# Optimization experiments

Measured on AMD Instinct MI355X. Metric: run time of the kernel, lower is better.

## Reference

```python
import jax, jax.numpy as jnp
import numpy as np
from jax import lax

B = 8          # batch
IMG = 224      # image size
PATCH = 16     # patch size / stride
D = 384        # embed_dim = d_model = d_inner (expand=1)
DEPTH = 24     # number of blocks
N = 16         # d_state
K = 4          # d_conv
R = 24         # dt_rank = ceil(D/16)
H = D * 4 * 2 // 3   # SwiGLU hidden = 1024
L = (IMG // PATCH) ** 2  # 196 tokens


def setup_inputs() -> dict:
    ks = iter(jax.random.split(jax.random.key(0), 40))
    def rn(shape, s=0.02):
        return jax.random.normal(next(ks), shape, jnp.float32) * s
    inp = {}
    inp["x"] = jax.random.normal(next(ks), (B, 3, IMG, IMG), jnp.float32)
    inp["patch_w"] = rn((D, 3, PATCH, PATCH))
    inp["patch_b"] = jnp.zeros((D,), jnp.float32)
    inp["norm1_w"] = jnp.ones((DEPTH, D), jnp.float32)
    inp["norm1_b"] = jnp.zeros((DEPTH, D), jnp.float32)
    inp["in_proj_w"] = rn((DEPTH, 2 * D, D))
    inp["conv_w"] = rn((DEPTH, D, K), 0.1)
    inp["conv_b"] = jnp.zeros((DEPTH, D), jnp.float32)
    inp["x_proj_w"] = rn((DEPTH, R + 2 * N, D))
    inp["dt_proj_w"] = rn((DEPTH, D, R), 0.1)
    inp["dt_proj_b"] = rn((DEPTH, D), 0.1)
    # S4D-real init: A = -exp(A_log), A_log = log(1..N)
    inp["A_log"] = jnp.tile(jnp.log(jnp.arange(1, N + 1, dtype=jnp.float32))[None, None, :], (DEPTH, D, 1))
    inp["D_skip"] = jnp.ones((DEPTH, D), jnp.float32)
    inp["out_proj_w"] = rn((DEPTH, D, D))
    inp["norm2_w"] = jnp.ones((DEPTH, D), jnp.float32)
    inp["norm2_b"] = jnp.zeros((DEPTH, D), jnp.float32)
    inp["w1_w"] = rn((DEPTH, H, D)); inp["w1_b"] = jnp.zeros((DEPTH, H), jnp.float32)
    inp["w2_w"] = rn((DEPTH, H, D)); inp["w2_b"] = jnp.zeros((DEPTH, H), jnp.float32)
    inp["w3_w"] = rn((DEPTH, D, H)); inp["w3_b"] = jnp.zeros((DEPTH, D), jnp.float32)
    inp["normf_w"] = jnp.ones((D,), jnp.float32)
    inp["normf_b"] = jnp.zeros((D,), jnp.float32)
    return inp


def _ln(x, w, b, eps=1e-5):
    m = x.mean(-1, keepdims=True)
    v = jnp.mean((x - m) ** 2, axis=-1, keepdims=True)
    return (x - m) / jnp.sqrt(v + eps) * w + b


def _mamba(x, in_w, cw, cb, xp_w, dtw, dtb, a_log, d_skip, ow):
    # x: [B, L, D]; Mamba with expand=1, bimamba 'none'
    bsz, seq, _ = x.shape
    xz = jnp.einsum('bld,ed->ble', x, in_w)        # [B, L, 2D]
    xc, z = jnp.split(xz, 2, axis=-1)
    # causal depthwise conv1d, kernel K, padding K-1, truncated to L
    xpd = jnp.pad(xc, ((0, 0), (K - 1, 0), (0, 0)))
    xconv = sum(xpd[:, k:k + seq, :] * cw[:, k] for k in range(K)) + cb
    xa = jax.nn.silu(xconv)
    dbc = jnp.einsum('bld,ed->ble', xa, xp_w)      # [B, L, R+2N]
    dt = jax.nn.softplus(jnp.einsum('blr,dr->bld', dbc[..., :R], dtw) + dtb)  # [B, L, D]
    Bm = dbc[..., R:R + N]                         # [B, L, N]
    Cm = dbc[..., R + N:]                          # [B, L, N]
    A = -jnp.exp(a_log)                            # [D, N]

    def step(h, t):
        dt_t, B_t, C_t, x_t = t                    # [B,D],[B,N],[B,N],[B,D]
        h = h * jnp.exp(dt_t[..., None] * A) + (dt_t * x_t)[..., None] * B_t[:, None, :]
        return h, jnp.einsum('bdn,bn->bd', h, C_t)

    h0 = jnp.zeros((bsz, D, N), x.dtype)
    _, ys = lax.scan(step, h0, (dt.transpose(1, 0, 2), Bm.transpose(1, 0, 2),
                                Cm.transpose(1, 0, 2), xa.transpose(1, 0, 2)))
    y = ys.transpose(1, 0, 2) + d_skip * xa
    y = y * jax.nn.silu(z)
    return jnp.einsum('bld,ed->ble', y, ow)


def _forward(x, patch_w, patch_b, norm1_w, norm1_b, in_proj_w, conv_w, conv_b,
             x_proj_w, dt_proj_w, dt_proj_b, A_log, D_skip, out_proj_w,
             norm2_w, norm2_b, w1_w, w1_b, w2_w, w2_b, w3_w, w3_b, normf_w, normf_b):
    p = lax.conv_general_dilated(x, patch_w, (PATCH, PATCH), 'VALID',
                                 dimension_numbers=('NCHW', 'OIHW', 'NCHW'))
    p = p + patch_b[None, :, None, None]
    h = p.reshape(p.shape[0], D, -1).transpose(0, 2, 1)   # [B, L, D]
    for i in range(DEPTH):
        h = h + _mamba(_ln(h, norm1_w[i], norm1_b[i]), in_proj_w[i], conv_w[i], conv_b[i],
                       x_proj_w[i], dt_proj_w[i], dt_proj_b[i], A_log[i], D_skip[i], out_proj_w[i])
        hn = _ln(h, norm2_w[i], norm2_b[i])
        hid = jax.nn.silu(hn @ w1_w[i].T + w1_b[i]) * (hn @ w2_w[i].T + w2_b[i])
        h = h + hid @ w3_w[i].T + w3_b[i]
    return _ln(h, normf_w, normf_b)


def reference(x, patch_w, patch_b, norm1_w, norm1_b, in_proj_w, conv_w, conv_b,
              x_proj_w, dt_proj_w, dt_proj_b, A_log, D_skip, out_proj_w,
              norm2_w, norm2_b, w1_w, w1_b, w2_w, w2_b, w3_w, w3_b, normf_w, normf_b):
    return _forward(x, patch_w, patch_b, norm1_w, norm1_b, in_proj_w, conv_w, conv_b,
                    x_proj_w, dt_proj_w, dt_proj_b, A_log, D_skip, out_proj_w,
                    norm2_w, norm2_b, w1_w, w1_b, w2_w, w2_b, w3_w, w3_b, normf_w, normf_b)
```

## Files before the change

kernel.cpp:

```cpp
#include <hip/hip_runtime.h>
#include <math.h>

#define BB 8
#define LL 196
#define DD 384
#define NDEPTH 24
#define NST 16
#define RRANK 24
#define HHID 1024
#define MROWS (BB*LL)
#define NCH 28
#define CHL 7

typedef float f32x4 __attribute__((ext_vector_type(4)));
typedef short s16x8 __attribute__((ext_vector_type(8)));
typedef short s16x4 __attribute__((ext_vector_type(4)));
typedef __bf16 b16x8 __attribute__((ext_vector_type(8)));
typedef unsigned short u16;
typedef unsigned int u32;

#if defined(__has_builtin)
#  if __has_builtin(__builtin_amdgcn_global_load_lds)
#    define HAS_GLL 1
#  endif
#endif
#ifndef HAS_GLL
#  define HAS_GLL 0
#endif

__device__ __forceinline__ float sigmoidf_(float x){ return 1.f/(1.f+__expf(-x)); }

__device__ __forceinline__ u16 f2bf(float f){
    u32 u = __builtin_bit_cast(u32, f);
    u32 r = (u + 0x7fffu + ((u >> 16) & 1u)) >> 16;
    return (u16)r;
}
__device__ __forceinline__ float bf2f(u16 v){
    u32 u = ((u32)v) << 16;
    return __builtin_bit_cast(float, u);
}

__device__ __forceinline__ void gll16(const u16* g, void* lds){
#if HAS_GLL
    __builtin_amdgcn_global_load_lds(
        (const __attribute__((address_space(1))) unsigned int*)g,
        (__attribute__((address_space(3))) unsigned int*)lds, 16, 0, 0);
#endif
}

template<int N> __device__ __forceinline__ void waitbar(){
    if constexpr (N==0) asm volatile("s_waitcnt vmcnt(0) lgkmcnt(0)\ns_barrier" ::: "memory");
    else if constexpr (N==4) asm volatile("s_waitcnt vmcnt(4) lgkmcnt(0)\ns_barrier" ::: "memory");
    else if constexpr (N==8) asm volatile("s_waitcnt vmcnt(8) lgkmcnt(0)\ns_barrier" ::: "memory");
    else asm volatile("s_waitcnt vmcnt(0) lgkmcnt(0)\ns_barrier" ::: "memory");
    __builtin_amdgcn_sched_barrier(0);
}
__device__ __forceinline__ void bar_release(){
    asm volatile("s_waitcnt lgkmcnt(0)\ns_barrier" ::: "memory");
    __builtin_amdgcn_sched_barrier(0);
}

template<typename V>
__device__ __forceinline__ auto mfma_try(V a, V b, f32x4 c, int)
    -> decltype(__builtin_amdgcn_mfma_f32_16x16x32_bf16(a, b, c, 0, 0, 0))
{ return __builtin_amdgcn_mfma_f32_16x16x32_bf16(a, b, c, 0, 0, 0); }

template<typename V>
__device__ __forceinline__ f32x4 mfma_try(V a, V b, f32x4 c, long)
{
    return __builtin_amdgcn_mfma_f32_16x16x32_bf16(
        __builtin_bit_cast(b16x8, a), __builtin_bit_cast(b16x8, b), c, 0, 0, 0);
}
__device__ __forceinline__ f32x4 mfma_bf16(s16x8 a, s16x8 b, f32x4 c){ return mfma_try(a, b, c, 0); }

__global__ __launch_bounds__(64) void ln_k(const float* __restrict__ X,
    const float* __restrict__ w, const float* __restrict__ b, float* __restrict__ Y)
{
    int row = blockIdx.x;
    int lane = threadIdx.x;
    const float* x = X + (size_t)row*DD;
    float v[6]; float s=0.f, s2=0.f;
    #pragma unroll
    for (int j=0;j<6;j++){ float t = x[lane + j*64]; v[j]=t; s+=t; s2+=t*t; }
    #pragma unroll
    for (int o=32;o>=1;o>>=1){ s += __shfl_xor(s,o); s2 += __shfl_xor(s2,o); }
    float m = s*(1.f/DD);
    float var = s2*(1.f/DD) - m*m;
    float rstd = rsqrtf(var + 1e-5f);
    #pragma unroll
    for (int j=0;j<6;j++){
        int c = lane + j*64;
        Y[(size_t)row*DD + c] = (v[j]-m)*rstd*w[c] + b[c];
    }
}

__global__ void gather_k(const float* __restrict__ x, u16* __restrict__ P)
{
    int idx = blockIdx.x*blockDim.x + threadIdx.x;
    if (idx >= MROWS*768) return;
    int k = idx % 768;
    int bl = idx / 768;
    int l = bl % LL;
    int b = bl / LL;
    int c = k >> 8;
    int rem = k & 255;
    int dy = rem >> 4, dx = rem & 15;
    int py = l / 14, px = l % 14;
    P[idx] = f2bf(x[(((size_t)b*3 + c)*224 + (py*16+dy))*224 + (px*16+dx)]);
}

__device__ __forceinline__ int swz(int row, int chunk){
    return (row << 7) + ((chunk ^ (row & 7)) << 4);
}

template<int EPI, bool WB, int CFG, int PRO, int K>
__global__ __launch_bounds__(256) void mgemm_k(
    const u16* __restrict__ A, const float* __restrict__ Af,
    const float* __restrict__ lnw, const float* __restrict__ lnb,
    const void* __restrict__ W1v, const void* __restrict__ W2v,
    const float* __restrict__ bias1, const float* __restrict__ bias2,
    float* __restrict__ Cf, u16* __restrict__ Cb,
    int M, int N)
{
    constexpr int  BM   = (CFG==1)?32:16;
    constexpr int  FM   = (CFG==2)?1:2;
    constexpr int  FN   = 2;
    constexpr int  NAR  = (BM+31)/32;
    constexpr bool DUAL = (EPI==4);
    constexpr bool RES  = (EPI==2 || EPI==3);
    constexpr int  ABY  = BM*128;
    constexpr int  BBY  = 128*128;
    constexpr bool ASY  = WB && (HAS_GLL==1);
    constexpr int  NKT  = K >> 6;
    constexpr int  NLW  = DUAL ? 8 : 4;
    __shared__ __attribute__((aligned(16))) char sm[2*ABY + 2*BBY + (DUAL ? 2*BBY : 0)];
    char* A0 = sm;          char* A1 = sm + ABY;
    char* B0 = sm + 2*ABY;  char* B1 = B0 + BBY;
    char* C0 = B1 + BBY;    char* C1 = C0 + BBY;

    const int tid = threadIdx.x;
    const int row0 = blockIdx.y * BM;
    const int col0 = blockIdx.x << 7;
    const int w = tid >> 6, lane = tid & 63;
    const int wn  = w;
    const int lr = lane & 15, lk = lane >> 4;
    const int ar0 = tid >> 3, ac8 = tid & 7;
    const bool apart = (CFG != 2) || (tid < 128);

    const u16*   W1b = (const u16*)W1v;
    const u16*   W2b = (const u16*)W2v;
    const float* W1f = (const float*)W1v;
    const float* W2f = (const float*)W2v;

    f32x4 acc [FM][FN] = {};
    f32x4 acc2[FM][FN] = {};

    float cres[FM][FN][4];
    if (RES){
        #pragma unroll
        for (int n=0;n<FN;n++){
            int gc = col0 + wn*32 + n*16 + lr;
            #pragma unroll
            for (int m=0;m<FM;m++){
                #pragma unroll
                for (int r=0;r<4;r++){
                    int gr = row0 + m*16 + lk*4 + r;
                    cres[m][n][r] = (gc < N && gr < M) ? Cf[(size_t)gr*N + gc] : 0.f;
                }
            }
        }
    }

    s16x8 aval[NAR];
    s16x8 bval[4], b2val[4];
    float4 bvf[8], b2vf[8];
    s16x8 lnr[(PRO==1)?NKT:1];

    if (PRO == 1 && apart){
        const float* xrow = Af + (size_t)(row0 + ar0)*DD;
        float4 va[6], vb[6];
        float s = 0.f, s2 = 0.f;
        #pragma unroll
        for (int j=0;j<6;j++){
            va[j] = *(const float4*)(xrow + j*64 + ac8*8);
            vb[j] = *(const float4*)(xrow + j*64 + ac8*8 + 4);
            s  += va[j].x+va[j].y+va[j].z+va[j].w + vb[j].x+vb[j].y+vb[j].z+vb[j].w;
            s2 += va[j].x*va[j].x+va[j].y*va[j].y+va[j].z*va[j].z+va[j].w*va[j].w
                + vb[j].x*vb[j].x+vb[j].y*vb[j].y+vb[j].z*vb[j].z+vb[j].w*vb[j].w;
        }
        #pragma unroll
        for (int o=1;o<8;o<<=1){ s += __shfl_xor(s,o); s2 += __shfl_xor(s2,o); }
        float m = s*(1.f/DD);
        float rstd = rsqrtf(s2*(1.f/DD) - m*m + 1e-5f);
        #pragma unroll
        for (int j=0;j<6;j++){
            int c0 = j*64 + ac8*8;
            float4 w0 = *(const float4*)(lnw + c0);
            float4 w1 = *(const float4*)(lnw + c0 + 4);
            float4 b0 = *(const float4*)(lnb + c0);
            float4 b1 = *(const float4*)(lnb + c0 + 4);
            s16x8 ov;
            ov[0]=(short)f2bf((va[j].x-m)*rstd*w0.x+b0.x);
            ov[1]=(short)f2bf((va[j].y-m)*rstd*w0.y+b0.y);
            ov[2]=(short)f2bf((va[j].z-m)*rstd*w0.z+b0.z);
            ov[3]=(short)f2bf((va[j].w-m)*rstd*w0.w+b0.w);
            ov[4]=(short)f2bf((vb[j].x-m)*rstd*w1.x+b1.x);
            ov[5]=(short)f2bf((vb[j].y-m)*rstd*w1.y+b1.y);
            ov[6]=(short)f2bf((vb[j].z-m)*rstd*w1.z+b1.z);
            ov[7]=(short)f2bf((vb[j].w-m)*rstd*w1.w+b1.w);
            if (j < NKT) lnr[j] = ov;
        }
    }

    auto stageAsync = [&](int kt, char* bA, char* bB, char* bC){
        const int lhi = lane >> 3, llo = lane & 7;
        const int colel = (kt << 6) + ((llo ^ lhi) << 3);
        if (PRO == 0){
            constexpr int ACH = BM/8;
            #pragma unroll
            for (int ci = w; ci < ACH; ci += 4){
                int gr = row0 + ci*8 + lhi;
                gll16(A + (size_t)gr*K + colel, bA + ci*1024);
            }
        }
        #pragma unroll
        for (int i=0;i<4;i++){
            int ci = w*4 + i;
            int gb = col0 + ci*8 + lhi;
            gll16(W1b + (size_t)gb*K + colel, bB + ci*1024);
        }
        if (DUAL){
            #pragma unroll
            for (int i=0;i<4;i++){
                int ci = w*4 + i;
                int gb = col0 + ci*8 + lhi;
                gll16(W2b + (size_t)gb*K + colel, bC + ci*1024);
            }
        }
    };

    auto loadT = [&](int kt){
        const int kb = kt << 6;
        if (PRO == 0 && apart){
            #pragma unroll
            for (int i=0;i<NAR;i++){
                int gr = row0 + i*32 + ar0;
                if (gr < M) aval[i] = *(const s16x8*)(A + (size_t)gr*K + kb + ac8*8);
                else        aval[i] = s16x8{0,0,0,0,0,0,0,0};
            }
        }
        if (WB){
            #pragma unroll
            for (int i=0;i<4;i++){
                int gb = col0 + i*32 + ar0;
                if (gb < N) bval[i] = *(const s16x8*)(W1b + (size_t)gb*K + kb + ac8*8);
                else        bval[i] = s16x8{0,0,0,0,0,0,0,0};
            }
            if (DUAL){
                #pragma unroll
                for (int i=0;i<4;i++){
                    int gb = col0 + i*32 + ar0;
                    if (gb < N) b2val[i] = *(const s16x8*)(W2b + (size_t)gb*K + kb + ac8*8);
                    else        b2val[i] = s16x8{0,0,0,0,0,0,0,0};
                }
            }
        } else {
            #pragma unroll
            for (int i=0;i<8;i++){
                int ss = i*256 + tid;
                int r = ss >> 4, q = ss & 15;
                int gb = col0 + r;
                if (gb < N) bvf[i] = *(const float4*)(W1f + (size_t)gb*K + kb + q*4);
                else        bvf[i] = float4{0,0,0,0};
            }
            if (DUAL){
                #pragma unroll
                for (int i=0;i<8;i++){
                    int ss = i*256 + tid;
                    int r = ss >> 4, q = ss & 15;
                    int gb = col0 + r;
                    if (gb < N) b2vf[i] = *(const float4*)(W2f + (size_t)gb*K + kb + q*4);
                    else        b2vf[i] = float4{0,0,0,0};
                }
            }
        }
    };
    auto writeT = [&](char* bA, char* bB, char* bC){
        if (PRO == 0 && apart){
            #pragma unroll
            for (int i=0;i<NAR;i++)
                *(s16x8*)(bA + swz(i*32 + ar0, ac8)) = aval[i];
        }
        if (WB){
            #pragma unroll
            for (int i=0;i<4;i++)
                *(s16x8*)(bB + swz(i*32 + ar0, ac8)) = bval[i];
            if (DUAL){
                #pragma unroll
                for (int i=0;i<4;i++)
                    *(s16x8*)(bC + swz(i*32 + ar0, ac8)) = b2val[i];
            }
        } else {
            #pragma unroll
            for (int i=0;i<8;i++){
                int ss = i*256 + tid;
                int r = ss >> 4, q = ss & 15;
                float4 v = bvf[i];
                s16x4 cv = { (short)f2bf(v.x), (short)f2bf(v.y), (short)f2bf(v.z), (short)f2bf(v.w) };
                int off = (r << 7) + (((q >> 1) ^ (r & 7)) << 4) + ((q & 1) << 3);
                *(s16x4*)(bB + off) = cv;
            }
            if (DUAL){
                #pragma unroll
                for (int i=0;i<8;i++){
                    int ss = i*256 + tid;
                    int r = ss >> 4, q = ss & 15;
                    float4 v = b2vf[i];
                    s16x4 cv = { (short)f2bf(v.x), (short)f2bf(v.y), (short)f2bf(v.z), (short)f2bf(v.w) };
                    int off = (r << 7) + (((q >> 1) ^ (r & 7)) << 4) + ((q & 1) << 3);
                    *(s16x4*)(bC + off) = cv;
                }
            }
        }
    };

    auto compute = [&](char* cA, char* cB, char* cC){
        #pragma unroll
        for (int ks=0; ks<2; ks++){
            s16x8 af[FM], bfr[FN];
            #pragma unroll
            for (int m=0;m<FM;m++)
                af[m] = *(const s16x8*)(cA + swz(m*16 + lr, ks*4 + lk));
            #pragma unroll
            for (int n=0;n<FN;n++)
                bfr[n] = *(const s16x8*)(cB + swz(wn*32 + n*16 + lr, ks*4 + lk));
            #pragma unroll
            for (int m=0;m<FM;m++)
                #pragma unroll
                for (int n=0;n<FN;n++)
                    acc[m][n] = mfma_bf16(af[m], bfr[n], acc[m][n]);
            if (DUAL){
                s16x8 b2r[FN];
                #pragma unroll
                for (int n=0;n<FN;n++)
                    b2r[n] = *(const s16x8*)(cC + swz(wn*32 + n*16 + lr, ks*4 + lk));
                #pragma unroll
                for (int m=0;m<FM;m++)
                    #pragma unroll
                    for (int n=0;n<FN;n++)
                        acc2[m][n] = mfma_bf16(af[m], b2r[n], acc2[m][n]);
            }
        }
    };

    if (ASY){
        stageAsync(0, A0, B0, C0);
        if (NKT > 1) stageAsync(1, A1, B1, C1);
        if (PRO == 1 && apart){
            *(s16x8*)(A0 + swz(ar0, ac8)) = lnr[0];
            if (NKT > 1) *(s16x8*)(A1 + swz(ar0, ac8)) = lnr[(1 < NKT) ? 1 : 0];
        }
        if (NKT > 1) waitbar<NLW>(); else waitbar<0>();
        #pragma unroll
        for (int kt=0; kt<NKT; kt++){
            if (kt & 1) compute(A1, B1, C1);
            else        compute(A0, B0, C0);
            if (kt+1 < NKT){
                bar_release();
                if (kt+2 < NKT){
                    char* rA = (kt&1)?A1:A0; char* rB = (kt&1)?B1:B0; char* rC = (kt&1)?C1:C0;
                    stageAsync(kt+2, rA, rB, rC);
                    if (PRO == 1 && apart)
                        *(s16x8*)(rA + swz(ar0, ac8)) = lnr[(kt+2 < NKT) ? (kt+2) : 0];
                    waitbar<NLW>();
                } else {
                    waitbar<0>();
                }
            }
        }
    } else {
        loadT(0); writeT(A0, B0, C0);
        if (PRO == 1 && apart) *(s16x8*)(A0 + swz(ar0, ac8)) = lnr[0];
        __syncthreads();
        #pragma unroll
        for (int kt=0; kt<NKT; kt++){
            const bool more = (kt+1 < NKT);
            char* nA = (kt&1)?A0:A1; char* nB = (kt&1)?B0:B1; char* nC = (kt&1)?C0:C1;
            if (more){
                loadT(kt+1);
                if (PRO == 1 && apart) *(s16x8*)(nA + swz(ar0, ac8)) = lnr[(kt+1 < NKT) ? (kt+1) : 0];
            }
            if (kt & 1) compute(A1, B1, C1);
            else        compute(A0, B0, C0);
            if (more) writeT(nA, nB, nC);
            __syncthreads();
        }
    }

    #pragma unroll
    for (int n=0;n<FN;n++){
        int gc = col0 + wn*32 + n*16 + lr;
        if (gc >= N) continue;
        float b1 = 0.f, b2 = 0.f;
        if (EPI==1||EPI==3||EPI==4) b1 = bias1[gc];
        if (EPI==4) b2 = bias2[gc];
        #pragma unroll
        for (int m=0;m<FM;m++){
            #pragma unroll
            for (int r=0;r<4;r++){
                int gr = row0 + m*16 + lk*4 + r;
                if (gr >= M) continue;
                float v = acc[m][n][r];
                if (EPI==1||EPI==3) v += b1;
                if (RES) v += cres[m][n][r];
                if (EPI==4){
                    float v1 = v + b1;
                    float v2 = acc2[m][n][r] + b2;
                    Cb[(size_t)gr*N + gc] = f2bf(v1 * sigmoidf_(v1) * v2);
                } else if (EPI==6){
                    Cb[(size_t)gr*N + gc] = f2bf(v);
                } else {
                    Cf[(size_t)gr*N + gc] = v;
                }
            }
        }
    }
}

__global__ void cvtw_k(const float* __restrict__ s, u16* __restrict__ d, int n)
{
    int i = blockIdx.x*blockDim.x + threadIdx.x;
    int idx = i*4;
    if (idx + 4 <= n){
        float4 v = *(const float4*)(s + idx);
        s16x4 cv = { (short)f2bf(v.x), (short)f2bf(v.y), (short)f2bf(v.z), (short)f2bf(v.w) };
        *(s16x4*)(d + idx) = cv;
    } else {
        for (int j=idx;j<n;j++) d[j] = f2bf(s[j]);
    }
}

__global__ __launch_bounds__(384) void scanA_k(
    const float* __restrict__ Wx, const u16* __restrict__ xzb,
    const float* __restrict__ cw, const float* __restrict__ cb,
    const float* __restrict__ dtw, const float* __restrict__ dtb,
    const float* __restrict__ a_log,
    float* __restrict__ Pout, float* __restrict__ Sout,
    float2* __restrict__ dtxv, float* __restrict__ dbc)
{
    __shared__ float xaS[CHL][DD+4];
    __shared__ float Ds[CHL][56];
    int b = blockIdx.x / NCH;
    int c = blockIdx.x % NCH;
    int d = threadIdx.x;

    float cwr[4];
    #pragma unroll
    for (int k=0;k<4;k++) cwr[k] = cw[d*4+k];
    float cbv = cb[d];
    int l0 = c*CHL;
    float p3=0.f, p2=0.f, p1=0.f;
    if (l0 >= 3) p3 = bf2f(xzb[(size_t)(b*LL+l0-3)*768 + d]);
    if (l0 >= 2) p2 = bf2f(xzb[(size_t)(b*LL+l0-2)*768 + d]);
    if (l0 >= 1) p1 = bf2f(xzb[(size_t)(b*LL+l0-1)*768 + d]);
    float xv[CHL];
    #pragma unroll
    for (int j=0;j<CHL;j++){
        int row = b*LL + l0 + j;
        float cur = bf2f(xzb[(size_t)row*768 + d]);
        float a = cbv;
        a = fmaf(p3, cwr[0], a); a = fmaf(p2, cwr[1], a);
        a = fmaf(p1, cwr[2], a); a = fmaf(cur, cwr[3], a);
        p3 = p2; p2 = p1; p1 = cur;
        xv[j] = a * sigmoidf_(a);
        xaS[j][d] = xv[j];
    }
    __syncthreads();

    for (int t = d; t < CHL*56; t += 384){
        int q = t / CHL, j = t - q*CHL;
        const float* Wr = Wx + (size_t)q*DD;
        float accd = 0.f;
        #pragma unroll 8
        for (int dd=0; dd<DD; dd+=4){
            float4 wv = *(const float4*)(Wr + dd);
            accd = fmaf(xaS[j][dd],   wv.x, accd);
            accd = fmaf(xaS[j][dd+1], wv.y, accd);
            accd = fmaf(xaS[j][dd+2], wv.z, accd);
            accd = fmaf(xaS[j][dd+3], wv.w, accd);
        }
        Ds[j][q] = accd;
        dbc[(size_t)(b*LL + l0 + j)*56 + q] = accd;
    }
    __syncthreads();

    float dtwr[RRANK];
    #pragma unroll
    for (int r=0;r<RRANK;r++) dtwr[r] = dtw[d*RRANK + r];
    float dtbv = dtb[d];
    float Aa[NST];
    #pragma unroll
    for (int n=0;n<NST;n++) Aa[n] = -__expf(a_log[d*NST+n]);
    float hst[NST], P[NST];
    #pragma unroll
    for (int n=0;n<NST;n++){ hst[n]=0.f; P[n]=1.f; }
    #pragma unroll
    for (int j=0;j<CHL;j++){
        int row = b*LL + l0 + j;
        float t = dtbv;
        #pragma unroll
        for (int r=0;r<RRANK;r++) t = fmaf(dtwr[r], Ds[j][r], t);
        float dtv = (t > 20.f) ? t : log1pf(__expf(t));
        dtxv[(size_t)row*DD + d] = float2{dtv, xv[j]};
        float du = dtv*xv[j];
        #pragma unroll
        for (int n=0;n<NST;n++){
            float e = __expf(dtv*Aa[n]);
            hst[n] = fmaf(hst[n], e, du*Ds[j][24+n]);
            P[n] *= e;
        }
    }
    size_t base = ((size_t)(b*NCH + c)*DD + d)*NST;
    #pragma unroll
    for (int n=0;n<NST;n++){ Pout[base+n]=P[n]; Sout[base+n]=hst[n]; }
}

__global__ __launch_bounds__(256) void scanB_k(
    const float* __restrict__ P, const float* __restrict__ S,
    float* __restrict__ Hin)
{
    int t = blockIdx.x*blockDim.x + threadIdx.x;
    if (t >= BB*DD*NST) return;
    int n = t % NST;
    int d = (t / NST) % DD;
    int b = t / (NST*DD);
    float h = 0.f;
    for (int c=0; c<NCH; c++){
        size_t idx = ((size_t)(b*NCH + c)*DD + d)*NST + n;
        Hin[idx] = h;
        h = fmaf(P[idx], h, S[idx]);
    }
}

__global__ __launch_bounds__(384) void scanC_k(
    const float* __restrict__ dbc, const float2* __restrict__ dtxv,
    const u16* __restrict__ xzb, const float* __restrict__ a_log,
    const float* __restrict__ Hin,
    const float* __restrict__ dskip,
    u16* __restrict__ yg)
{
    int b = blockIdx.x / NCH;
    int c = blockIdx.x % NCH;
    int d = threadIdx.x;
    __shared__ float Ds[CHL][56];
    for (int t = threadIdx.x; t < CHL*56; t += 384){
        int j = t/56, q = t%56;
        Ds[j][q] = dbc[(size_t)(b*LL + c*CHL + j)*56 + q];
    }
    __syncthreads();
    float hst[NST];
    size_t hb = ((size_t)(b*NCH + c)*DD + d)*NST;
    #pragma unroll
    for (int n=0;n<NST;n++) hst[n] = Hin[hb+n];
    float Aa[NST];
    #pragma unroll
    for (int n=0;n<NST;n++) Aa[n] = -__expf(a_log[d*NST+n]);
    float dsk = dskip[d];
    int l0 = c*CHL;
    #pragma unroll
    for (int j=0;j<CHL;j++){
        int row = b*LL + l0 + j;
        float2 dx = dtxv[(size_t)row*DD + d];
        float dtv = dx.x, xv = dx.y;
        float du = dtv*xv;
        float y = 0.f;
        #pragma unroll
        for (int n=0;n<NST;n++){
            float e = __expf(dtv*Aa[n]);
            hst[n] = fmaf(hst[n], e, du*Ds[j][24+n]);
            y = fmaf(hst[n], Ds[j][40+n], y);
        }
        float zv = bf2f(xzb[(size_t)row*768 + 384 + d]);
        float g = zv * sigmoidf_(zv);
        yg[(size_t)row*DD + d] = f2bf((y + dsk*xv)*g);
    }
}

template<int EPI, int CFG, int PRO, int K>
static void mg(bool wb, dim3 g, hipStream_t s,
               const void* A, const float* Af, const float* lnw, const float* lnb,
               const void* Wb, const void* Wf, const void* W2b, const void* W2f,
               const float* b1, const float* b2, float* Cf, u16* Cb,
               int M, int N)
{
    if (wb) mgemm_k<EPI,true ,CFG,PRO,K><<<g,256,0,s>>>((const u16*)A, Af, lnw, lnb, Wb, W2b, b1, b2, Cf, Cb, M, N);
    else    mgemm_k<EPI,false,CFG,PRO,K><<<g,256,0,s>>>((const u16*)A, Af, lnw, lnb, Wf, W2f, b1, b2, Cf, Cb, M, N);
}

extern "C" void kernel_launch(void* const* d_in, const int* in_sizes, int n_in,
                              void* d_out, int out_size, void* d_ws, size_t ws_size,
                              hipStream_t stream)
{
    const float* x         = (const float*)d_in[0];
    const float* patch_w   = (const float*)d_in[1];
    const float* patch_b   = (const float*)d_in[2];
    const float* norm1_w   = (const float*)d_in[3];
    const float* norm1_b   = (const float*)d_in[4];
    const float* in_proj_w = (const float*)d_in[5];
    const float* conv_w    = (const float*)d_in[6];
    const float* conv_b    = (const float*)d_in[7];
    const float* x_proj_w  = (const float*)d_in[8];
    const float* dt_w      = (const float*)d_in[9];
    const float* dt_b      = (const float*)d_in[10];
    const float* A_log     = (const float*)d_in[11];
    const float* D_skip    = (const float*)d_in[12];
    const float* out_w     = (const float*)d_in[13];
    const float* norm2_w   = (const float*)d_in[14];
    const float* norm2_b   = (const float*)d_in[15];
    const float* w1_w      = (const float*)d_in[16];
    const float* w1_b      = (const float*)d_in[17];
    const float* w2_w      = (const float*)d_in[18];
    const float* w2_b      = (const float*)d_in[19];
    const float* w3_w      = (const float*)d_in[20];
    const float* w3_b      = (const float*)d_in[21];
    const float* normf_w   = (const float*)d_in[22];
    const float* normf_b   = (const float*)d_in[23];

    char* wsb = (char*)d_ws;
    size_t o = 0;
    auto take = [&](size_t bytes) -> char* {
        char* p = wsb + o;
        o += (bytes + 255) & ~(size_t)255;
        return p;
    };

    float* h    = (float*)take((size_t)602112*4);
    float* dbc  = (float*)take((size_t)87808*4);
    float* Pb   = (float*)take((size_t)BB*NCH*DD*NST*4);
    float* Sb   = (float*)take((size_t)BB*NCH*DD*NST*4);
    float* Hi   = (float*)take((size_t)BB*NCH*DD*NST*4);
    float2* dtxv= (float2*)take((size_t)MROWS*DD*8);
    u16*  xzb   = (u16*)take((size_t)1204224*2);
    u16*  yg    = (u16*)take((size_t)602112*2);
    u16*  hid   = (u16*)take((size_t)1605632*2);
    u16*  patches = hid;

    const size_t NPW = 294912, NIN = 7077888, NOUT = 3538944,
                 NW1 = 9437184, NW2 = 9437184, NW3 = 9437184;
    u16* wcP = (u16*)take(NPW*2);
    u16* wcI = (u16*)take(NIN*2);
    u16* wcO = (u16*)take(NOUT*2);
    u16* wc1 = (u16*)take(NW1*2);
    u16* wc2 = (u16*)take(NW2*2);
    u16* wc3 = (u16*)take(NW3*2);
    bool wb = (ws_size >= o);

    if (wb){
        cvtw_k<<<(int)((NPW/4+255)/256), 256, 0, stream>>>(patch_w, wcP, (int)NPW);
        cvtw_k<<<(int)((NIN/4+255)/256), 256, 0, stream>>>(in_proj_w, wcI, (int)NIN);
        cvtw_k<<<(int)((NOUT/4+255)/256),256, 0, stream>>>(out_w, wcO, (int)NOUT);
        cvtw_k<<<(int)((NW1/4+255)/256), 256, 0, stream>>>(w1_w, wc1, (int)NW1);
        cvtw_k<<<(int)((NW2/4+255)/256), 256, 0, stream>>>(w2_w, wc2, (int)NW2);
        cvtw_k<<<(int)((NW3/4+255)/256), 256, 0, stream>>>(w3_w, wc3, (int)NW3);
    }

    const int GY32 = MROWS/32;
    const int GY16 = MROWS/16;

    gather_k<<<(MROWS*768+255)/256, 256, 0, stream>>>(x, patches);
    mg<1,2,0,768>(wb, dim3(3,GY16), stream, patches, nullptr, nullptr, nullptr,
              wcP, patch_w, nullptr, nullptr, patch_b, nullptr, h, nullptr, MROWS, DD);

    for (int i=0;i<NDEPTH;i++){
        mg<6,1,1,384>(wb, dim3(6,GY32), stream, nullptr, h, norm1_w + i*DD, norm1_b + i*DD,
                  wcI + (size_t)i*768*DD, in_proj_w + (size_t)i*768*DD, nullptr, nullptr,
                  nullptr, nullptr, nullptr, xzb, MROWS, 768);
        scanA_k<<<BB*NCH, 384, 0, stream>>>(x_proj_w + (size_t)i*56*DD, xzb,
                                            conv_w + i*DD*4, conv_b + i*DD,
                                            dt_w + (size_t)i*DD*RRANK, dt_b + i*DD,
                                            A_log + (size_t)i*DD*NST, Pb, Sb, dtxv, dbc);
        scanB_k<<<(BB*DD*NST+255)/256, 256, 0, stream>>>(Pb, Sb, Hi);
        scanC_k<<<BB*NCH, 384, 0, stream>>>(dbc, dtxv, xzb, A_log + (size_t)i*DD*NST,
                                            Hi, D_skip + i*DD, yg);
        mg<2,2,0,384>(wb, dim3(3,GY16), stream, yg, nullptr, nullptr, nullptr,
                  wcO + (size_t)i*DD*DD, out_w + (size_t)i*DD*DD, nullptr, nullptr,
                  nullptr, nullptr, h, nullptr, MROWS, DD);
        mg<4,1,1,384>(wb, dim3(8,GY32), stream, nullptr, h, norm2_w + i*DD, norm2_b + i*DD,
                  wc1 + (size_t)i*HHID*DD, w1_w + (size_t)i*HHID*DD,
                  wc2 + (size_t)i*HHID*DD, w2_w + (size_t)i*HHID*DD,
                  w1_b + i*HHID, w2_b + i*HHID, nullptr, hid, MROWS, HHID);
        mg<3,2,0,1024>(wb, dim3(3,GY16), stream, hid, nullptr, nullptr, nullptr,
                  wc3 + (size_t)i*DD*HHID, w3_w + (size_t)i*DD*HHID, nullptr, nullptr,
                  w3_b + i*DD, nullptr, h, nullptr, MROWS, DD);
    }

    ln_k<<<MROWS, 64, 0, stream>>>(h, normf_w, normf_b, (float*)d_out);
}
```

Baseline: 1.963 ms.

## Fuse out_proj GEMM into scan output kernel with fp32 FMA

Removes the separate out_proj MFMA GEMM launch by having each scanC block keep its 7-row y*gate tile in shared memory and compute the 384x384 projection with scalar fp32 FMAs, adding the result straight into the residual h. Out_proj weights are pre-transposed into an interleaved fp32 layout so each thread reads float4 weights coalesced. This saves a launch and the bf16 yg round trip through global memory. In exchange, every block re-reads the full fp32 weight matrix, and the projection runs on vector ALUs instead of matrix cores.

```diff
diff --git a/kernel.cpp b/kernel.cpp
--- a/kernel.cpp
+++ b/kernel.cpp
@@ -440,6 +440,17 @@
     }
 }
 
+__global__ void cvtP_k(const float* __restrict__ s, float* __restrict__ d)
+{
+    int idx = blockIdx.x*blockDim.x + threadIdx.x;
+    if (idx >= NDEPTH*DD*DD) return;
+    int q   = idx & 3;
+    int e   = (idx >> 2) % DD;
+    int dd4 = ((idx >> 2) / DD) % (DD/4);
+    int L   = idx / (DD*DD);
+    d[idx] = s[(size_t)L*DD*DD + (size_t)e*DD + dd4*4 + q];
+}
+
 __global__ __launch_bounds__(384) void scanA_k(
     const float* __restrict__ Wx, const u16* __restrict__ xzb,
     const float* __restrict__ cw, const float* __restrict__ cb,
@@ -542,17 +553,19 @@
     }
 }
 
+template<int FUSE>
 __global__ __launch_bounds__(384) void scanC_k(
     const float* __restrict__ dbc, const float2* __restrict__ dtxv,
     const u16* __restrict__ xzb, const float* __restrict__ a_log,
     const float* __restrict__ Hin,
-    const float* __restrict__ dskip,
-    u16* __restrict__ yg)
-{
+    const float* __restrict__ dskip, const float* __restrict__ Wp,
+    float* __restrict__ h, u16* __restrict__ yg)
+{
+    __shared__ float ygS[CHL][DD+4];
+    __shared__ float Ds[CHL][56];
     int b = blockIdx.x / NCH;
     int c = blockIdx.x % NCH;
     int d = threadIdx.x;
-    __shared__ float Ds[CHL][56];
     for (int t = threadIdx.x; t < CHL*56; t += 384){
         int j = t/56, q = t%56;
         Ds[j][q] = dbc[(size_t)(b*LL + c*CHL + j)*56 + q];
@@ -582,7 +595,32 @@
         }
         float zv = bf2f(xzb[(size_t)row*768 + 384 + d]);
         float g = zv * sigmoidf_(zv);
-        yg[(size_t)row*DD + d] = f2bf((y + dsk*xv)*g);
+        float yv = (y + dsk*xv)*g;
+        if (FUSE) ygS[j][d] = yv;
+        else      yg[(size_t)row*DD + d] = f2bf(yv);
+    }
+    if (FUSE){
+        __syncthreads();
+        float o[CHL];
+        #pragma unroll
+        for (int j=0;j<CHL;j++) o[j] = 0.f;
+        #pragma unroll 4
+        for (int dd4=0; dd4<DD/4; dd4++){
+            float4 wv = *(const float4*)(Wp + ((size_t)dd4*DD + d)*4);
+            int dd = dd4*4;
+            #pragma unroll
+            for (int j=0;j<CHL;j++){
+                o[j] = fmaf(ygS[j][dd],   wv.x, o[j]);
+                o[j] = fmaf(ygS[j][dd+1], wv.y, o[j]);
+                o[j] = fmaf(ygS[j][dd+2], wv.z, o[j]);
+                o[j] = fmaf(ygS[j][dd+3], wv.w, o[j]);
+            }
+        }
+        #pragma unroll
+        for (int j=0;j<CHL;j++){
+            size_t idx = (size_t)(b*LL + l0 + j)*DD + d;
+            h[idx] += o[j];
+        }
     }
 }
 
@@ -647,21 +685,21 @@
 
     const size_t NPW = 294912, NIN = 7077888, NOUT = 3538944,
                  NW1 = 9437184, NW2 = 9437184, NW3 = 9437184;
-    u16* wcP = (u16*)take(NPW*2);
-    u16* wcI = (u16*)take(NIN*2);
-    u16* wcO = (u16*)take(NOUT*2);
-    u16* wc1 = (u16*)take(NW1*2);
-    u16* wc2 = (u16*)take(NW2*2);
-    u16* wc3 = (u16*)take(NW3*2);
+    u16*   wcP = (u16*)take(NPW*2);
+    u16*   wcI = (u16*)take(NIN*2);
+    u16*   wc1 = (u16*)take(NW1*2);
+    u16*   wc2 = (u16*)take(NW2*2);
+    u16*   wc3 = (u16*)take(NW3*2);
+    float* wpO = (float*)take(NOUT*4);
     bool wb = (ws_size >= o);
 
     if (wb){
         cvtw_k<<<(int)((NPW/4+255)/256), 256, 0, stream>>>(patch_w, wcP, (int)NPW);
         cvtw_k<<<(int)((NIN/4+255)/256), 256, 0, stream>>>(in_proj_w, wcI, (int)NIN);
-        cvtw_k<<<(int)((NOUT/4+255)/256),256, 0, stream>>>(out_w, wcO, (int)NOUT);
         cvtw_k<<<(int)((NW1/4+255)/256), 256, 0, stream>>>(w1_w, wc1, (int)NW1);
         cvtw_k<<<(int)((NW2/4+255)/256), 256, 0, stream>>>(w2_w, wc2, (int)NW2);
         cvtw_k<<<(int)((NW3/4+255)/256), 256, 0, stream>>>(w3_w, wc3, (int)NW3);
+        cvtP_k<<<(int)((NOUT+255)/256), 256, 0, stream>>>(out_w, wpO);
     }
 
     const int GY32 = MROWS/32;
@@ -680,11 +718,18 @@
                                             dt_w + (size_t)i*DD*RRANK, dt_b + i*DD,
                                             A_log + (size_t)i*DD*NST, Pb, Sb, dtxv, dbc);
         scanB_k<<<(BB*DD*NST+255)/256, 256, 0, stream>>>(Pb, Sb, Hi);
-        scanC_k<<<BB*NCH, 384, 0, stream>>>(dbc, dtxv, xzb, A_log + (size_t)i*DD*NST,
-                                            Hi, D_skip + i*DD, yg);
-        mg<2,2,0,384>(wb, dim3(3,GY16), stream, yg, nullptr, nullptr, nullptr,
-                  wcO + (size_t)i*DD*DD, out_w + (size_t)i*DD*DD, nullptr, nullptr,
-                  nullptr, nullptr, h, nullptr, MROWS, DD);
+        if (wb){
+            scanC_k<1><<<BB*NCH, 384, 0, stream>>>(dbc, dtxv, xzb, A_log + (size_t)i*DD*NST,
+                                                   Hi, D_skip + i*DD,
+                                                   wpO + (size_t)i*DD*DD, h, nullptr);
+        } else {
+            scanC_k<0><<<BB*NCH, 384, 0, stream>>>(dbc, dtxv, xzb, A_log + (size_t)i*DD*NST,
+                                                   Hi, D_skip + i*DD,
+                                                   nullptr, nullptr, yg);
+            mg<2,2,0,384>(false, dim3(3,GY16), stream, yg, nullptr, nullptr, nullptr,
+                      nullptr, out_w + (size_t)i*DD*DD, nullptr, nullptr,
+                      nullptr, nullptr, h, nullptr, MROWS, DD);
+        }
         mg<4,1,1,384>(wb, dim3(8,GY32), stream, nullptr, h, norm2_w + i*DD, norm2_b + i*DD,
                   wc1 + (size_t)i*HHID*DD, w1_w + (size_t)i*HHID*DD,
                   wc2 + (size_t)i*HHID*DD, w2_w + (size_t)i*HHID*DD,
```

Result: slower. 2.682 ms (+36.7%).
